# Optimization experiments

Hardware: AMD Instinct MI355X
Metric: run time of the kernel (lower is better)

Reference implementation:

```python
import jax, jax.numpy as jnp
import numpy as np

# Dimensions (Tacotron2-style decoder)
B, T_ENC, T_MEL, N_MEL = 32, 400, 800, 80
ENC_DIM = 768          # encoder(512) + token(256) + speaker(0)
PRENET, ATT_RNN, DEC_RNN = 256, 1024, 1024
ATT_DIM, LOC_FILT, LOC_K = 128, 32, 31


def setup_inputs() -> dict:
    key = jax.random.key(0)
    ks = iter(jax.random.split(key, 32))
    def lin(shape):  # weight stored [out, in(,k)], scaled by 1/sqrt(fan_in)
        fan_in = int(np.prod(shape[1:])) if len(shape) > 1 else shape[0]
        return jax.random.normal(next(ks), shape, jnp.float32) / np.sqrt(fan_in)
    return {
        'memory': jax.random.normal(next(ks), (B, T_ENC, ENC_DIM), jnp.float32),
        'decoder_inputs': jax.random.normal(next(ks), (B, N_MEL, T_MEL), jnp.float32),
        'f0s': jnp.zeros((B, 1, T_MEL), jnp.float32),  # include_f0=False -> unused
        'prenet_w1': lin((PRENET, N_MEL)),
        'prenet_w2': lin((PRENET, PRENET)),
        'att_wih': lin((4 * ATT_RNN, PRENET + ENC_DIM)),
        'att_whh': lin((4 * ATT_RNN, ATT_RNN)),
        'att_bih': jnp.zeros((4 * ATT_RNN,), jnp.float32),
        'att_bhh': jnp.zeros((4 * ATT_RNN,), jnp.float32),
        'q_w': lin((ATT_DIM, ATT_RNN)),
        'mem_w': lin((ATT_DIM, ENC_DIM)),
        'v_w': lin((ATT_DIM,)),
        'loc_conv_w': lin((LOC_FILT, 2, LOC_K)),
        'loc_dense_w': lin((ATT_DIM, LOC_FILT)),
        'dec_wih': lin((4 * DEC_RNN, ATT_RNN + ENC_DIM)),
        'dec_whh': lin((4 * DEC_RNN, DEC_RNN)),
        'dec_bih': jnp.zeros((4 * DEC_RNN,), jnp.float32),
        'dec_bhh': jnp.zeros((4 * DEC_RNN,), jnp.float32),
        'proj_w': lin((N_MEL, DEC_RNN + ENC_DIM)),
        'proj_b': jnp.zeros((N_MEL,), jnp.float32),
        'gate_w': lin((DEC_RNN + ENC_DIM,)),
        'gate_b': jnp.zeros((), jnp.float32),
        'memory_lengths': jax.random.randint(next(ks), (B,), T_ENC // 2, T_ENC + 1),
    }


def _lstm_cell(x, h, c, wih, whh, bih, bhh):
    g = x @ wih.T + bih + h @ whh.T + bhh
    i, f, gg, o = jnp.split(g, 4, axis=-1)  # torch LSTMCell gate order i,f,g,o
    c = jax.nn.sigmoid(f) * c + jax.nn.sigmoid(i) * jnp.tanh(gg)
    h = jax.nn.sigmoid(o) * jnp.tanh(c)
    return h, c


def reference(memory, decoder_inputs, f0s, prenet_w1, prenet_w2,
              att_wih, att_whh, att_bih, att_bhh, q_w, mem_w, v_w,
              loc_conv_w, loc_dense_w, dec_wih, dec_whh, dec_bih, dec_bhh,
              proj_w, proj_b, gate_w, gate_b, memory_lengths):
    # include_f0=False: f0s ignored. Dropout disabled (p=0, deterministic),
    # p_teacher_forcing=1.0 -> always teacher-force, n_frames_per_step=1.
    mask = jnp.arange(T_ENC)[None, :] >= memory_lengths[:, None]  # [B,T_enc]
    pmem = jnp.einsum('bte,ae->bta', memory, mem_w)               # processed_memory

    # parse_decoder_inputs + go frame + prenet (teacher-forced inputs)
    frames = jnp.transpose(decoder_inputs, (2, 0, 1))             # [T_mel,B,N_MEL]
    frames = jnp.concatenate([jnp.zeros((1, B, N_MEL), frames.dtype), frames], 0)
    pre = jax.nn.relu(frames @ prenet_w1.T)
    pre = jax.nn.relu(pre @ prenet_w2.T)                          # [T_mel+1,B,PRENET]
    xs = pre[:T_MEL]

    def step(carry, x):
        ah, ac, dh, dc, aw, awc, ctx = carry
        ah, ac = _lstm_cell(jnp.concatenate([x, ctx], -1), ah, ac,
                            att_wih, att_whh, att_bih, att_bhh)
        awcat = jnp.stack([aw, awc], axis=1)                      # [B,2,T_enc]
        loc = jax.lax.conv_general_dilated(
            awcat, loc_conv_w, (1,), [(LOC_K // 2, LOC_K // 2)],
            dimension_numbers=('NCH', 'OIH', 'NCH'))              # [B,LOC_FILT,T_enc]
        ploc = jnp.einsum('bft,af->bta', loc, loc_dense_w)        # [B,T_enc,ATT_DIM]
        pq = ah @ q_w.T                                           # [B,ATT_DIM]
        e = jnp.tanh(pq[:, None, :] + pmem + ploc) @ v_w          # [B,T_enc]
        e = jnp.where(mask, -1e9, e)
        aw = jax.nn.softmax(e, axis=-1)
        ctx = jnp.einsum('bt,bte->be', aw, memory)
        awc = awc + aw
        dh, dc = _lstm_cell(jnp.concatenate([ah, ctx], -1), dh, dc,
                            dec_wih, dec_whh, dec_bih, dec_bhh)
        dha = jnp.concatenate([dh, ctx], axis=1)
        mel = dha @ proj_w.T + proj_b                             # [B,N_MEL]
        gate = dha @ gate_w + gate_b                              # [B]
        return (ah, ac, dh, dc, aw, awc, ctx), (mel, gate, aw)

    f32 = memory.dtype
    carry0 = (jnp.zeros((B, ATT_RNN), f32), jnp.zeros((B, ATT_RNN), f32),
              jnp.zeros((B, DEC_RNN), f32), jnp.zeros((B, DEC_RNN), f32),
              jnp.zeros((B, T_ENC), f32), jnp.zeros((B, T_ENC), f32),
              jnp.zeros((B, ENC_DIM), f32))
    _, (mels, gates, aligns) = jax.lax.scan(step, carry0, xs)
    mel_outputs = jnp.transpose(mels, (1, 2, 0))                  # [B,N_MEL,T_mel]
    gate_outputs = gates.T                                        # [B,T_mel]
    alignments = jnp.transpose(aligns, (1, 0, 2))                 # [B,T_mel,T_enc]
    return mel_outputs, gate_outputs, alignments
```

## Files before the change

kernel.cpp:

```cpp
#include <hip/hip_runtime.h>
#include <hip/hip_fp16.h>
#include <math.h>

#define TENC 400
#define TMEL 800
#define NMEL 80
#define ENCD 768
#define PRE  256
#define ARNN 1024
#define DRNN 1024
#define ATTD 128
#define NBLK 256
#define SLOT 32

typedef unsigned uint32;

__device__ __forceinline__ float4 ld4(const float* p){ return *(const float4*)p; }
__device__ __forceinline__ float sigmf(float x){ return 1.f/(1.f + __expf(-x)); }

__device__ __forceinline__ float ld_c(const float* p){
  union { unsigned u; float f; } c;
  c.u = __hip_atomic_load((const unsigned*)p, __ATOMIC_RELAXED, __HIP_MEMORY_SCOPE_AGENT);
  return c.f;
}
__device__ __forceinline__ void st_c(float* p, float v){
  union { unsigned u; float f; } c; c.f = v;
  __hip_atomic_store((unsigned*)p, c.u, __ATOMIC_RELAXED, __HIP_MEMORY_SCOPE_AGENT);
}
__device__ __forceinline__ float4 ld4_c(const float* p){
  union { unsigned long long u[2]; float4 f; } c;
  c.u[0] = __hip_atomic_load((const unsigned long long*)p, __ATOMIC_RELAXED,
                             __HIP_MEMORY_SCOPE_AGENT);
  c.u[1] = __hip_atomic_load((const unsigned long long*)(p+2), __ATOMIC_RELAXED,
                             __HIP_MEMORY_SCOPE_AGENT);
  return c.f;
}
__device__ __forceinline__ void st2_c(float* p, float a, float b){
  union { unsigned long long u; float f[2]; } c; c.f[0]=a; c.f[1]=b;
  __hip_atomic_store((unsigned long long*)p, c.u, __ATOMIC_RELAXED,
                     __HIP_MEMORY_SCOPE_AGENT);
}
__device__ __forceinline__ uint32 ald(const uint32* p){
  return __hip_atomic_load(p, __ATOMIC_RELAXED, __HIP_MEMORY_SCOPE_AGENT);
}
__device__ __forceinline__ void ast(uint32* p, uint32 v){
  __hip_atomic_store(p, v, __ATOMIC_RELAXED, __HIP_MEMORY_SCOPE_AGENT);
}

__device__ __forceinline__ void xbar(uint32* arr, uint32* relx, uint32 ph,
                                     int xcc, int role)
{
  __syncthreads();
  int tid = threadIdx.x;
  if (tid == 0) {
    asm volatile("s_waitcnt vmcnt(0)" ::: "memory");
    ast(arr + (xcc*32 + role)*SLOT, ph);
  }
  __syncthreads();
  if (role == 0) {
    if (tid < 32) {
      while (ald(arr + (xcc*32 + tid)*SLOT) < ph) __builtin_amdgcn_s_sleep(1);
    }
    __syncthreads();
    if (tid == 0) ast(relx + xcc*SLOT, ph);
  } else if (tid == 0) {
    while (ald(relx + xcc*SLOT) < ph) __builtin_amdgcn_s_sleep(1);
  }
  __syncthreads();
}

__device__ __forceinline__ void gbar8(uint32* arr, uint32* relg, uint32 ph,
                                      int xcc, int role)
{
  __syncthreads();
  int tid = threadIdx.x;
  int bl = role >> 3;
  if (tid == 0) {
    asm volatile("s_waitcnt vmcnt(0)" ::: "memory");
    ast(arr + (xcc*32 + role)*SLOT, ph);
  }
  __syncthreads();
  if ((role & 7) == 0) {
    if (tid < 8) {
      while (ald(arr + (xcc*32 + bl*8 + tid)*SLOT) < ph) __builtin_amdgcn_s_sleep(1);
    }
    __syncthreads();
    if (tid == 0) ast(relg + (xcc*4 + bl)*SLOT, ph);
  } else if (tid == 0) {
    while (ald(relg + (xcc*4 + bl)*SLOT) < ph) __builtin_amdgcn_s_sleep(1);
  }
  __syncthreads();
}

__global__ __launch_bounds__(256) void prenet_kernel(
    const float* __restrict__ din, const float* __restrict__ w1,
    const float* __restrict__ w2, float* __restrict__ xsT)
{
  int t = blockIdx.x;
  __shared__ float f_s[32*80];
  __shared__ float p_s[32*257];
  for (int id = threadIdx.x; id < 32*80; id += 256) {
    int b = id / 80, m = id - b*80;
    f_s[id] = (t == 0) ? 0.f : din[b*(NMEL*TMEL) + m*TMEL + (t-1)];
  }
  __syncthreads();
  for (int b = 0; b < 32; ++b) {
    int k = threadIdx.x;
    float acc = 0.f;
    #pragma unroll 4
    for (int m = 0; m < 80; ++m) acc += f_s[b*80+m] * w1[k*80+m];
    p_s[b*257+k] = fmaxf(acc, 0.f);
  }
  __syncthreads();
  int b = threadIdx.x & 31, jslot = threadIdx.x >> 5;
  for (int jj = 0; jj < 32; ++jj) {
    int j = jslot*32 + jj;
    const float* w2r = w2 + j*256;
    float acc = 0.f;
    #pragma unroll 4
    for (int kk = 0; kk < 256; ++kk) acc += p_s[b*257+kk] * w2r[kk];
    xsT[(size_t)t*8192 + j*32 + b] = fmaxf(acc, 0.f);
  }
}

__global__ __launch_bounds__(256) void pmem_kernel(
  const float* __restrict__ mem, const float* __restrict__ mw, __half* __restrict__ pm16)
{
  int b = blockIdx.y, tc = blockIdx.x;
  int a = threadIdx.x & 127, th = threadIdx.x >> 7;
  for (int i = 0; i < 8; ++i) {
    int tt = tc*16 + th + 2*i;
    const float* mrow = mem + (size_t)b*(TENC*ENCD) + (size_t)tt*ENCD;
    const float* wrow = mw + a*ENCD;
    float acc = 0.f;
    #pragma unroll 4
    for (int e4 = 0; e4 < ENCD; e4 += 4) {
      float4 mv = ld4(mrow+e4), wv = ld4(wrow+e4);
      acc += mv.x*wv.x + mv.y*wv.y + mv.z*wv.z + mv.w*wv.w;
    }
    pm16[b*(TENC*ATTD) + tt*ATTD + a] = __float2half(acc);
  }
}

__global__ __launch_bounds__(256) void cvt16_kernel(
  const float* __restrict__ src, __half* __restrict__ dst, int n)
{
  int i = blockIdx.x*256 + threadIdx.x;
  int st = gridDim.x*256;
  for (; i < n; i += st) dst[i] = __float2half(src[i]);
}

struct DecArgs {
  const float *xsT;
  const __half *awih16, *awhh16, *dwih16, *dwhh16, *qw16, *pm16;
  const float *abih, *abhh, *dbih, *dbhh;
  const float *cw, *ldw, *vw;
  const int*  mlen;
  const float *pw, *pb, *gw, *gb;
  const float *memory;
  float *ahX, *dhX, *ctxX, *awX, *awcX, *eX;
  float *out_mel, *out_gate, *out_align;
  uint32 *roleCtr, *arr, *relx, *relg;
};


template<int KIH>
__device__ __forceinline__ void dmaW(const __half* __restrict__ wih,
                                     const __half* __restrict__ whh,
                                     int g, int u0g, int c, char* slot, int lane)
{
  const int kk = c*128;
  const __half* base = (kk < KIH) ? wih : whh;
  const int kbase = (kk < KIH) ? kk : (kk - KIH);
  const size_t kstr = (kk < KIH) ? (size_t)KIH : (size_t)1024;
  const int r = lane >> 4, kp = lane & 15;
  const __half* src = base + (size_t)(g*1024 + u0g + r)*kstr + kbase + kp*8;
  #pragma unroll
  for (int i = 0; i < 8; ++i) {
    __builtin_amdgcn_global_load_lds(
      (const __attribute__((address_space(1))) void*)(src + (size_t)(i*4)*kstr),
      (__attribute__((address_space(3))) void*)(slot + i*1024), 16, 0, 0);
  }
}

template<int E0, int E1, bool S0W>
__device__ __forceinline__ void loadX(int c, int lane, int b0,
  const float* __restrict__ s0, const float* __restrict__ s1,
  const float* __restrict__ s2, float4& xlo, float4& xhi)
{
  int k0 = c*128 + lane*2;
  if (S0W && c < E0) {
    xlo = ld4_c(s0 + (size_t)k0*32 + b0);
    xhi = ld4_c(s0 + (size_t)(k0+1)*32 + b0);
  } else if (c < E0) {
    xlo = ld4_c(s0 + (size_t)k0*4);
    xhi = ld4_c(s0 + (size_t)k0*4 + 4);
  } else if (c < E1) {
    int kb = k0 - E0*128;
    xlo = ld4_c(s1 + (size_t)kb*4);
    xhi = ld4_c(s1 + (size_t)kb*4 + 4);
  } else {
    int kb = k0 - E1*128;
    xlo = ld4_c(s2 + (size_t)kb*4);
    xhi = ld4_c(s2 + (size_t)kb*4 + 4);
  }
}

__device__ __forceinline__ void compW(const char* slot, int lane,
                                      float4 xlo, float4 xhi, float* acc)
{
  #pragma unroll
  for (int u = 0; u < 32; ++u) {
    __half2 w2 = *(const __half2*)(slot + u*256 + lane*4);
    float2 wf = __half22float2(w2);
    acc[u*4+0] += wf.x*xlo.x + wf.y*xhi.x;
    acc[u*4+1] += wf.x*xlo.y + wf.y*xhi.y;
    acc[u*4+2] += wf.x*xlo.z + wf.y*xhi.z;
    acc[u*4+3] += wf.x*xlo.w + wf.y*xhi.w;
  }
}

#define RS_ROUND(m, n) { bool hi = (lane & m) != 0; \
  _Pragma("unroll") for (int i = 0; i < n; ++i) { \
    float v = hi ? acc[i] : acc[i+n]; \
    float o = __shfl_xor(v, m); \
    acc[i] = (hi ? acc[i+n] : acc[i]) + o; } }

#define SBAR() __builtin_amdgcn_sched_barrier(0)
#define WAITV12() { asm volatile("s_waitcnt vmcnt(12)" ::: "memory"); SBAR(); }
#define WAITV0()  { asm volatile("s_waitcnt vmcnt(0)"  ::: "memory"); SBAR(); }
#define WAITL0()  { asm volatile("s_waitcnt lgkmcnt(0)" ::: "memory"); SBAR(); }

template<int NC, int E0, int E1, int KIH, bool S0W>
__device__ void gemm_stream(const __half* __restrict__ wih,
                            const __half* __restrict__ whh,
                            int u0g, int b0,
                            const float* __restrict__ s0,
                            const float* __restrict__ s1,
                            const float* __restrict__ s2,
                            char* ringAll, float* G)
{
  const int tid = threadIdx.x;
  const int g = tid >> 6, lane = tid & 63;
  char* slot0 = ringAll + g*16384;
  char* slot1 = slot0 + 8192;
  float acc[128];
  #pragma unroll
  for (int i = 0; i < 128; ++i) acc[i] = 0.f;

  float4 xa0, xa1, xb0, xb1;
  dmaW<KIH>(wih, whh, g, u0g, 0, slot0, lane); SBAR();
  loadX<E0,E1,S0W>(0, lane, b0, s0, s1, s2, xa0, xa1); SBAR();
  dmaW<KIH>(wih, whh, g, u0g, 1, slot1, lane); SBAR();
  loadX<E0,E1,S0W>(1, lane, b0, s0, s1, s2, xb0, xb1); SBAR();

  #pragma unroll 1
  for (int c = 0; c + 2 < NC; c += 2) {
    WAITV12();
    compW(slot0, lane, xa0, xa1, acc);
    WAITL0();
    dmaW<KIH>(wih, whh, g, u0g, c+2, slot0, lane); SBAR();
    loadX<E0,E1,S0W>(c+2, lane, b0, s0, s1, s2, xa0, xa1); SBAR();
    WAITV12();
    compW(slot1, lane, xb0, xb1, acc);
    WAITL0();
    dmaW<KIH>(wih, whh, g, u0g, c+3, slot1, lane); SBAR();
    loadX<E0,E1,S0W>(c+3, lane, b0, s0, s1, s2, xb0, xb1); SBAR();
  }
  WAITV12();
  compW(slot0, lane, xa0, xa1, acc);
  WAITV0();
  compW(slot1, lane, xb0, xb1, acc);

  RS_ROUND(32,64) RS_ROUND(16,32) RS_ROUND(8,16)
  RS_ROUND(4,8)   RS_ROUND(2,4)   RS_ROUND(1,2)
  {
    int pidx = lane*2;
    int u = pidx >> 2, b = pidx & 3;
    *(float2*)(G + g*128 + u*4 + b) = make_float2(acc[0], acc[1]);
  }
}

__device__ __forceinline__ void cell_x(const float* G, int u0g,
  const float* __restrict__ bih, const float* __restrict__ bhh,
  float& creg, float* hbuf, float* __restrict__ hXw)
{
  int tid = threadIdx.x;
  __syncthreads();
  if (tid < 128) {
    int u = tid >> 2, b = tid & 3;
    int uu = u0g + u;
    float gi = G[0*128 + u*4+b] + bih[uu]        + bhh[uu];
    float gf = G[1*128 + u*4+b] + bih[1024+uu]   + bhh[1024+uu];
    float gg = G[2*128 + u*4+b] + bih[2048+uu]   + bhh[2048+uu];
    float go = G[3*128 + u*4+b] + bih[3072+uu]   + bhh[3072+uu];
    float cn = sigmf(gf)*creg + sigmf(gi)*tanhf(gg);
    creg = cn;
    hbuf[tid] = sigmf(go)*tanhf(cn);
  }
  __syncthreads();
  if (tid < 32) {
    float4 hv = *(float4*)(hbuf + tid*4);
    st2_c(hXw + (size_t)(u0g + tid)*4,     hv.x, hv.y);
    st2_c(hXw + (size_t)(u0g + tid)*4 + 2, hv.z, hv.w);
  }
  __syncthreads();
}

__device__ void proj_x(int role, int xcc, int t,
  const float* __restrict__ dhR, const float* __restrict__ ctxX, const DecArgs& p)
{
  int tid = threadIdx.x;
  int w = tid >> 6, lane = tid & 63;
  int base = role*10 + (role < 4 ? role : 4);
  int cnt  = (role < 4) ? 11 : 10;
  for (int i = w; i < cnt; i += 4) {
    int d = base + i;
    int bl = d / 81, r = d - bl*81;
    const float* wr = (r < 80) ? (p.pw + (size_t)r*1792) : p.gw;
    float a = 0.f;
    #pragma unroll 4
    for (int ii = 0; ii < 28; ++ii) {
      int k = lane + ii*64;
      float x = (k < 1024) ? ld_c(dhR + (size_t)k*4 + bl)
                           : ld_c(ctxX + (size_t)(k-1024)*4 + bl);
      a += x * wr[k];
    }
    #pragma unroll
    for (int m = 32; m >= 1; m >>= 1) a += __shfl_xor(a, m);
    if (lane == 0) {
      int b = xcc*4 + bl;
      if (r < 80) p.out_mel[((size_t)b*80 + r)*TMEL + t] = a + p.pb[r];
      else        p.out_gate[(size_t)b*TMEL + t]         = a + p.gb[0];
    }
  }
}

__device__ void energies_x(int bl, int c8, int xcc, const DecArgs& p,
  const float* __restrict__ ahW, const float* __restrict__ awXl,
  const float* __restrict__ awcXl, float* __restrict__ eXl, float* scr)
{
  int t0 = c8*50;
  float* ah_s  = scr;
  float* pq_s  = scr + 1024;
  float* part  = scr + 1152;
  float* aw_s  = scr + 1408;
  float* awc_s = scr + 1488;
  float* loc_s = scr + 1568;
  float* epart = scr + 3218;
  int tid = threadIdx.x;
  #pragma unroll
  for (int i = 0; i < 4; ++i) {
    int u = tid + i*256;
    ah_s[u] = ld_c(ahW + (size_t)u*4 + bl);
  }
  if (tid >= 96) {
    int i = tid - 96;
    int h = (i < 80) ? i : i - 80;
    bool isC = i >= 80;
    int gidx = t0 - 15 + h;
    float v = (gidx >= 0 && gidx < TENC)
            ? (isC ? ld_c(awcXl + gidx) : ld_c(awXl + gidx)) : 0.f;
    if (isC) awc_s[h] = v; else aw_s[h] = v;
  }
  __syncthreads();
  {
    int a = tid & 127, kh = tid >> 7;
    const __half* qr = p.qw16 + (size_t)a*1024 + kh*512;
    const float*  ar = ah_s + kh*512;
    float acc = 0.f;
    for (int k = 0; k < 512; k += 8) {
      uint4 hv = *(const uint4*)(qr + k);
      const __half2* h2 = (const __half2*)&hv;
      #pragma unroll
      for (int q = 0; q < 4; ++q) {
        float2 wf = __half22float2(h2[q]);
        acc += ar[k+q*2]*wf.x + ar[k+q*2+1]*wf.y;
      }
    }
    part[tid] = acc;
  }
  __syncthreads();
  if (tid < 128) pq_s[tid] = part[tid] + part[tid+128];
  for (int id = tid; id < 50*32; id += 256) {
    int tl = id >> 5, f = id & 31;
    const float* w0 = p.cw + f*62;
    float acc = 0.f;
    #pragma unroll
    for (int k = 0; k < 31; ++k)
      acc += aw_s[tl+k]*w0[k] + awc_s[tl+k]*w0[31+k];
    loc_s[tl*33 + f] = acc;
  }
  __syncthreads();
  if (tid < 200) {
    int tl = tid >> 2, qa = tid & 3;
    int tt = t0 + tl;
    const __half* pm = p.pm16 + (size_t)(xcc*4+bl)*(TENC*ATTD) + (size_t)tt*ATTD;
    float s = 0.f;
    for (int a = qa*32; a < qa*32 + 32; ++a) {
      const float* lw = p.ldw + a*32;
      float pl = 0.f;
      #pragma unroll 8
      for (int f = 0; f < 32; ++f) pl += loc_s[tl*33 + f] * lw[f];
      s += p.vw[a] * tanhf(pq_s[a] + __half2float(pm[a]) + pl);
    }
    epart[tl*4 + qa] = s;
  }
  __syncthreads();
  if (tid < 50) {
    int tt = t0 + tid;
    float v = epart[tid*4] + epart[tid*4+1] + epart[tid*4+2] + epart[tid*4+3];
    if (tt >= p.mlen[xcc*4+bl]) v = -1000000000.0f;
    st_c(eXl + tt, v);
  }
}

__device__ void smctx_x(int bl, int jc, int xcc, int t, const DecArgs& p,
  const float* __restrict__ eXl, float* __restrict__ awXl, float* __restrict__ awcXl,
  float* __restrict__ ctxX, const __half2* mem_s, float* scr)
{
  float* red   = scr;
  float* aw_s  = scr + 256;
  float* cpart = scr + 656;
  int tid = threadIdx.x;
  float v0 = ld_c(eXl + tid);
  float v1 = (tid + 256 < TENC) ? ld_c(eXl + tid + 256) : -3.0e38f;
  red[tid] = fmaxf(v0, v1); __syncthreads();
  for (int s = 128; s > 0; s >>= 1) {
    if (tid < s) red[tid] = fmaxf(red[tid], red[tid+s]);
    __syncthreads();
  }
  float mx = red[0]; __syncthreads();
  float p0 = __expf(v0 - mx);
  float p1 = (tid + 256 < TENC) ? __expf(v1 - mx) : 0.f;
  red[tid] = p0 + p1; __syncthreads();
  for (int s = 128; s > 0; s >>= 1) {
    if (tid < s) red[tid] += red[tid+s];
    __syncthreads();
  }
  float inv = 1.f / red[0];
  aw_s[tid] = p0 * inv;
  if (tid + 256 < TENC) aw_s[tid + 256] = p1 * inv;
  __syncthreads();
  if (tid < 192) {
    int jp = tid % 48, h = tid / 48;
    float ax = 0.f, ay = 0.f;
    for (int tt = h*100; tt < h*100 + 100; ++tt) {
      float av = aw_s[tt];
      float2 m = __half22float2(mem_s[tt*48 + jp]);
      ax += av * m.x; ay += av * m.y;
    }
    cpart[(h*48 + jp)*2]     = ax;
    cpart[(h*48 + jp)*2 + 1] = ay;
  }
  __syncthreads();
  if (tid < 48) {
    float sx = cpart[tid*2]        + cpart[(48+tid)*2]
             + cpart[(96+tid)*2]   + cpart[(144+tid)*2];
    float sy = cpart[tid*2+1]      + cpart[(48+tid)*2+1]
             + cpart[(96+tid)*2+1] + cpart[(144+tid)*2+1];
    int j = jc*96 + tid*2;
    st_c(ctxX + (size_t)j*4 + bl, sx);
    st_c(ctxX + (size_t)(j+1)*4 + bl, sy);
  }
  if (jc == 0) {
    for (int i = tid; i < TENC; i += 256) {
      float a = aw_s[i];
      st_c(awXl + i, a);
      st_c(awcXl + i, ld_c(awcXl + i) + a);
      p.out_align[((size_t)(xcc*4+bl)*TMEL + t)*TENC + i] = a;
    }
  }
}

__global__ __launch_bounds__(256, 1) void decoder_loop(DecArgs p)
{
  __shared__ __align__(16) char Wring[65536];
  __shared__ __half2 mem_s[400*48];
  __shared__ float G[512];
  __shared__ float hbuf[128];
  __shared__ int s_xcc, s_role;
  int tid = threadIdx.x;
  float* scr = (float*)Wring;

  if (tid == 0) {
    uint32 x;
    asm volatile("s_getreg_b32 %0, hwreg(HW_REG_XCC_ID)" : "=s"(x));
    int xc = (int)(x & 7);
    s_xcc = xc;
    s_role = (int)atomicAdd(&p.roleCtr[xc], 1u);
  }
  __syncthreads();
  const int xcc = s_xcc, role = s_role & 31;
  const int u0g = role*32;
  const int bl = role >> 3, jc = role & 7;
  const int b0 = xcc*4;

  float* ctxX  = p.ctxX + (size_t)xcc*3072;
  float* awXl  = p.awX  + (size_t)xcc*1600 + bl*400;
  float* awcXl = p.awcX + (size_t)xcc*1600 + bl*400;
  float* eXl   = p.eX   + (size_t)xcc*1600 + bl*400;

  {
    const float* mb = p.memory + (size_t)(b0+bl)*(TENC*ENCD);
    int j0 = jc*96;
    for (int idx = tid; idx < 400*48; idx += 256) {
      int tt = idx / 48, jp = idx - tt*48;
      mem_s[idx] = __floats2half2_rn(mb[(size_t)tt*ENCD + j0 + jp*2],
                                     mb[(size_t)tt*ENCD + j0 + jp*2 + 1]);
    }
  }
  float cA = 0.f, cD = 0.f;
  uint32 ph = 0;
  __syncthreads();

  for (int t = 0; t < TMEL; ++t) {
    const float* ahR = p.ahX + (size_t)((t+1)&1)*32768 + (size_t)xcc*4096;
    float*       ahW = p.ahX + (size_t)(t&1)*32768     + (size_t)xcc*4096;
    const float* dhR = p.dhX + (size_t)((t+1)&1)*32768 + (size_t)xcc*4096;
    float*       dhW = p.dhX + (size_t)(t&1)*32768     + (size_t)xcc*4096;

    if (t > 0) proj_x(role, xcc, t-1, dhR, ctxX, p);
    gemm_stream<16, 2, 8, 1024, true>(p.awih16, p.awhh16, u0g, b0,
        p.xsT + (size_t)t*8192, ctxX, ahR, Wring, G);
    cell_x(G, u0g, p.abih, p.abhh, cA, hbuf, ahW);
    xbar(p.arr, p.relx, ++ph, xcc, role);

    energies_x(bl, jc, xcc, p, ahW, awXl, awcXl, eXl, scr);
    gbar8(p.arr, p.relg, ++ph, xcc, role);

    smctx_x(bl, jc, xcc, t, p, eXl, awXl, awcXl, ctxX, mem_s, scr);
    xbar(p.arr, p.relx, ++ph, xcc, role);

    gemm_stream<22, 8, 14, 1792, false>(p.dwih16, p.dwhh16, u0g, 0,
        ahW, ctxX, dhR, Wring, G);
    cell_x(G, u0g, p.dbih, p.dbhh, cD, hbuf, dhW);
    xbar(p.arr, p.relx, ++ph, xcc, role);
  }

  proj_x(role, xcc, TMEL-1,
         p.dhX + (size_t)((TMEL-1)&1)*32768 + (size_t)xcc*4096, ctxX, p);
}

extern "C" void kernel_launch(void* const* d_in, const int* in_sizes, int n_in,
                              void* d_out, int out_size, void* d_ws, size_t ws_size,
                              hipStream_t stream)
{
  const float* memory = (const float*)d_in[0];
  const float* din    = (const float*)d_in[1];
  const float* w1     = (const float*)d_in[3];
  const float* w2     = (const float*)d_in[4];
  const float* awih   = (const float*)d_in[5];
  const float* awhh   = (const float*)d_in[6];
  const float* abih   = (const float*)d_in[7];
  const float* abhh   = (const float*)d_in[8];
  const float* q_w    = (const float*)d_in[9];
  const float* mem_w  = (const float*)d_in[10];
  const float* v_w    = (const float*)d_in[11];
  const float* cw     = (const float*)d_in[12];
  const float* ldw    = (const float*)d_in[13];
  const float* dwih   = (const float*)d_in[14];
  const float* dwhh   = (const float*)d_in[15];
  const float* dbih   = (const float*)d_in[16];
  const float* dbhh   = (const float*)d_in[17];
  const float* pw     = (const float*)d_in[18];
  const float* pb     = (const float*)d_in[19];
  const float* gw     = (const float*)d_in[20];
  const float* gb     = (const float*)d_in[21];
  const int*   mlen   = (const int*)d_in[22];

  float* p = (float*)d_ws;
  float* xsT    = p;              p += 800*256*32;
  __half* awih16 = (__half*)p;    p += 2097152;
  __half* awhh16 = (__half*)p;    p += 2097152;
  __half* dwih16 = (__half*)p;    p += 3670016;
  __half* dwhh16 = (__half*)p;    p += 2097152;
  __half* qw16   = (__half*)p;    p += 65536;
  __half* pm16   = (__half*)p;    p += 819200;
  float* zs      = p;
  uint32* roleCtr = (uint32*)p;   p += 8;
  uint32* arr    = (uint32*)p;    p += 256*SLOT;
  uint32* relx   = (uint32*)p;    p += 8*SLOT;
  uint32* relg   = (uint32*)p;    p += 32*SLOT;
  float* ahX     = p;             p += 2*8*1024*4;
  float* dhX     = p;             p += 2*8*1024*4;
  float* ctxX    = p;             p += 8*768*4;
  float* awX     = p;             p += 8*4*400;
  float* awcX    = p;             p += 8*4*400;
  float* eX      = p;             p += 8*4*400;
  size_t zcount  = (size_t)(p - zs);

  float* out_mel   = (float*)d_out;
  float* out_gate  = out_mel + 32*80*800;
  float* out_align = out_gate + 32*800;

  hipMemsetAsync(zs, 0, zcount*sizeof(float), stream);
  prenet_kernel<<<TMEL, 256, 0, stream>>>(din, w1, w2, xsT);
  pmem_kernel<<<dim3(25,32), 256, 0, stream>>>(memory, mem_w, pm16);
  cvt16_kernel<<<256, 256, 0, stream>>>(q_w, qw16, 128*1024);
  cvt16_kernel<<<2048, 256, 0, stream>>>(awih, awih16, 4096*1024);
  cvt16_kernel<<<2048, 256, 0, stream>>>(awhh, awhh16, 4096*1024);
  cvt16_kernel<<<2048, 256, 0, stream>>>(dwih, dwih16, 4096*1792);
  cvt16_kernel<<<2048, 256, 0, stream>>>(dwhh, dwhh16, 4096*1024);

  DecArgs a;
  a.xsT = xsT;
  a.awih16 = awih16; a.awhh16 = awhh16; a.dwih16 = dwih16; a.dwhh16 = dwhh16;
  a.qw16 = qw16; a.pm16 = pm16;
  a.abih = abih; a.abhh = abhh; a.dbih = dbih; a.dbhh = dbhh;
  a.cw = cw; a.ldw = ldw; a.vw = v_w; a.mlen = mlen;
  a.pw = pw; a.pb = pb; a.gw = gw; a.gb = gb;
  a.memory = memory;
  a.ahX = ahX; a.dhX = dhX; a.ctxX = ctxX; a.awX = awX; a.awcX = awcX; a.eX = eX;
  a.out_mel = out_mel; a.out_gate = out_gate; a.out_align = out_align;
  a.roleCtr = roleCtr; a.arr = arr; a.relx = relx; a.relg = relg;

  decoder_loop<<<NBLK, 256, 0, stream>>>(a);
}
```

Measured before the change: 113.8 ms.

## Triple-buffer LSTM weight and activation streaming via LDS DMA, move memory slice to global

The LSTM gemm stream changes from a two-slot ring with activation vectors in registers to a three-slot LDS ring. Both the fp16 weight chunk and the activation chunk are now fetched with global_load_lds, and the code waits on vmcnt before each compute step, so two chunks are in flight while one is consumed. To free LDS for the larger ring, the per-block half-precision memory slice is no longer staged in shared memory. A separate pre-kernel now writes it to global workspace, and the context computation reads it from global/L2 every step. The deeper prefetch is meant to hide weight-fetch latency. The cost is extra global traffic in the context stage and a relaxed-atomic load path replaced by plain DMA loads of cross-block data, whose coherence may differ.

New measurement: 130.8 ms. 1.15x slower.

```diff
diff --git a/kernel.cpp b/kernel.cpp
--- a/kernel.cpp
+++ b/kernel.cpp
@@ -26,14 +26,6 @@
 __device__ __forceinline__ void st_c(float* p, float v){
   union { unsigned u; float f; } c; c.f = v;
   __hip_atomic_store((unsigned*)p, c.u, __ATOMIC_RELAXED, __HIP_MEMORY_SCOPE_AGENT);
-}
-__device__ __forceinline__ float4 ld4_c(const float* p){
-  union { unsigned long long u[2]; float4 f; } c;
-  c.u[0] = __hip_atomic_load((const unsigned long long*)p, __ATOMIC_RELAXED,
-                             __HIP_MEMORY_SCOPE_AGENT);
-  c.u[1] = __hip_atomic_load((const unsigned long long*)(p+2), __ATOMIC_RELAXED,
-                             __HIP_MEMORY_SCOPE_AGENT);
-  return c.f;
 }
 __device__ __forceinline__ void st2_c(float* p, float a, float b){
   union { unsigned long long u; float f[2]; } c; c.f[0]=a; c.f[1]=b;
@@ -142,6 +134,19 @@
   }
 }
 
+__global__ __launch_bounds__(256) void mem16_kernel(
+  const float* __restrict__ mem, __half2* __restrict__ m16)
+{
+  int b = blockIdx.y, jc = blockIdx.x;
+  const float* mb = mem + (size_t)b*(TENC*ENCD) + jc*96;
+  __half2* dst = m16 + ((size_t)(b*8 + jc))*19200;
+  for (int idx = threadIdx.x; idx < 19200; idx += 256) {
+    int tt = idx / 48, jp = idx - tt*48;
+    dst[idx] = __floats2half2_rn(mb[(size_t)tt*ENCD + jp*2],
+                                 mb[(size_t)tt*ENCD + jp*2 + 1]);
+  }
+}
+
 __global__ __launch_bounds__(256) void cvt16_kernel(
   const float* __restrict__ src, __half* __restrict__ dst, int n)
 {
@@ -153,16 +158,21 @@
 struct DecArgs {
   const float *xsT;
   const __half *awih16, *awhh16, *dwih16, *dwhh16, *qw16, *pm16;
+  const __half2 *mem16;
   const float *abih, *abhh, *dbih, *dbhh;
   const float *cw, *ldw, *vw;
   const int*  mlen;
   const float *pw, *pb, *gw, *gb;
-  const float *memory;
   float *ahX, *dhX, *ctxX, *awX, *awcX, *eX;
   float *out_mel, *out_gate, *out_align;
   uint32 *roleCtr, *arr, *relx, *relg;
 };
 
+
+#define SBAR() __builtin_amdgcn_sched_barrier(0)
+#define WAITV20() { asm volatile("s_waitcnt vmcnt(20)" ::: "memory"); SBAR(); }
+#define WAITV10() { asm volatile("s_waitcnt vmcnt(10)" ::: "memory"); SBAR(); }
+#define WAITV0()  { asm volatile("s_waitcnt vmcnt(0)"  ::: "memory"); SBAR(); }
 
 template<int KIH>
 __device__ __forceinline__ void dmaW(const __half* __restrict__ wih,
@@ -184,31 +194,29 @@
 }
 
 template<int E0, int E1, bool S0W>
-__device__ __forceinline__ void loadX(int c, int lane, int b0,
+__device__ __forceinline__ void dmaX(int c, int lane, int b0,
   const float* __restrict__ s0, const float* __restrict__ s1,
-  const float* __restrict__ s2, float4& xlo, float4& xhi)
-{
-  int k0 = c*128 + lane*2;
-  if (S0W && c < E0) {
-    xlo = ld4_c(s0 + (size_t)k0*32 + b0);
-    xhi = ld4_c(s0 + (size_t)(k0+1)*32 + b0);
-  } else if (c < E0) {
-    xlo = ld4_c(s0 + (size_t)k0*4);
-    xhi = ld4_c(s0 + (size_t)k0*4 + 4);
-  } else if (c < E1) {
-    int kb = k0 - E0*128;
-    xlo = ld4_c(s1 + (size_t)kb*4);
-    xhi = ld4_c(s1 + (size_t)kb*4 + 4);
-  } else {
-    int kb = k0 - E1*128;
-    xlo = ld4_c(s2 + (size_t)kb*4);
-    xhi = ld4_c(s2 + (size_t)kb*4 + 4);
-  }
-}
-
-__device__ __forceinline__ void compW(const char* slot, int lane,
-                                      float4 xlo, float4 xhi, float* acc)
-{
+  const float* __restrict__ s2, char* slot)
+{
+  #pragma unroll
+  for (int j = 0; j < 2; ++j) {
+    int k = c*128 + j*64 + lane;
+    const float* src;
+    if (S0W && c < E0)      src = s0 + (size_t)k*32 + b0;
+    else if (c < E0)        src = s0 + (size_t)k*4;
+    else if (c < E1)        src = s1 + (size_t)(k - E0*128)*4;
+    else                    src = s2 + (size_t)(k - E1*128)*4;
+    __builtin_amdgcn_global_load_lds(
+      (const __attribute__((address_space(1))) void*)src,
+      (__attribute__((address_space(3))) void*)(slot + 8192 + j*1024 + lane*16),
+      16, 0, 1);
+  }
+}
+
+__device__ __forceinline__ void compW(const char* slot, int lane, float* acc)
+{
+  float4 xlo = *(const float4*)(slot + 8192 + lane*32);
+  float4 xhi = *(const float4*)(slot + 8192 + lane*32 + 16);
   #pragma unroll
   for (int u = 0; u < 32; ++u) {
     __half2 w2 = *(const __half2*)(slot + u*256 + lane*4);
@@ -226,11 +234,6 @@
     float o = __shfl_xor(v, m); \
     acc[i] = (hi ? acc[i+n] : acc[i]) + o; } }
 
-#define SBAR() __builtin_amdgcn_sched_barrier(0)
-#define WAITV12() { asm volatile("s_waitcnt vmcnt(12)" ::: "memory"); SBAR(); }
-#define WAITV0()  { asm volatile("s_waitcnt vmcnt(0)"  ::: "memory"); SBAR(); }
-#define WAITL0()  { asm volatile("s_waitcnt lgkmcnt(0)" ::: "memory"); SBAR(); }
-
 template<int NC, int E0, int E1, int KIH, bool S0W>
 __device__ void gemm_stream(const __half* __restrict__ wih,
                             const __half* __restrict__ whh,
@@ -242,35 +245,34 @@
 {
   const int tid = threadIdx.x;
   const int g = tid >> 6, lane = tid & 63;
-  char* slot0 = ringAll + g*16384;
-  char* slot1 = slot0 + 8192;
+  char* ring = ringAll + g*30720;
   float acc[128];
   #pragma unroll
   for (int i = 0; i < 128; ++i) acc[i] = 0.f;
 
-  float4 xa0, xa1, xb0, xb1;
-  dmaW<KIH>(wih, whh, g, u0g, 0, slot0, lane); SBAR();
-  loadX<E0,E1,S0W>(0, lane, b0, s0, s1, s2, xa0, xa1); SBAR();
-  dmaW<KIH>(wih, whh, g, u0g, 1, slot1, lane); SBAR();
-  loadX<E0,E1,S0W>(1, lane, b0, s0, s1, s2, xb0, xb1); SBAR();
-
+  dmaW<KIH>(wih, whh, g, u0g, 0, ring, lane);
+  dmaX<E0,E1,S0W>(0, lane, b0, s0, s1, s2, ring);
+  dmaW<KIH>(wih, whh, g, u0g, 1, ring + 10240, lane);
+  dmaX<E0,E1,S0W>(1, lane, b0, s0, s1, s2, ring + 10240);
+  SBAR();
+
+  int sc = 0, sp = 2;
   #pragma unroll 1
-  for (int c = 0; c + 2 < NC; c += 2) {
-    WAITV12();
-    compW(slot0, lane, xa0, xa1, acc);
-    WAITL0();
-    dmaW<KIH>(wih, whh, g, u0g, c+2, slot0, lane); SBAR();
-    loadX<E0,E1,S0W>(c+2, lane, b0, s0, s1, s2, xa0, xa1); SBAR();
-    WAITV12();
-    compW(slot1, lane, xb0, xb1, acc);
-    WAITL0();
-    dmaW<KIH>(wih, whh, g, u0g, c+3, slot1, lane); SBAR();
-    loadX<E0,E1,S0W>(c+3, lane, b0, s0, s1, s2, xb0, xb1); SBAR();
-  }
-  WAITV12();
-  compW(slot0, lane, xa0, xa1, acc);
-  WAITV0();
-  compW(slot1, lane, xb0, xb1, acc);
+  for (int c = 0; c < NC; ++c) {
+    if (c + 2 < NC) {
+      char* ps = ring + sp*10240;
+      dmaW<KIH>(wih, whh, g, u0g, c+2, ps, lane);
+      dmaX<E0,E1,S0W>(c+2, lane, b0, s0, s1, s2, ps);
+      SBAR();
+    }
+    if (c + 2 < NC)      { WAITV20(); }
+    else if (c + 1 < NC) { WAITV10(); }
+    else                 { WAITV0();  }
+    compW(ring + sc*10240, lane, acc);
+    SBAR();
+    sc = (sc+1 == 3) ? 0 : sc+1;
+    sp = (sp+1 == 3) ? 0 : sp+1;
+  }
 
   RS_ROUND(32,64) RS_ROUND(16,32) RS_ROUND(8,16)
   RS_ROUND(4,8)   RS_ROUND(2,4)   RS_ROUND(1,2)
@@ -417,7 +419,7 @@
 
 __device__ void smctx_x(int bl, int jc, int xcc, int t, const DecArgs& p,
   const float* __restrict__ eXl, float* __restrict__ awXl, float* __restrict__ awcXl,
-  float* __restrict__ ctxX, const __half2* mem_s, float* scr)
+  float* __restrict__ ctxX, const __half2* __restrict__ mslice, float* scr)
 {
   float* red   = scr;
   float* aw_s  = scr + 256;
@@ -447,7 +449,7 @@
     float ax = 0.f, ay = 0.f;
     for (int tt = h*100; tt < h*100 + 100; ++tt) {
       float av = aw_s[tt];
-      float2 m = __half22float2(mem_s[tt*48 + jp]);
+      float2 m = __half22float2(mslice[tt*48 + jp]);
       ax += av * m.x; ay += av * m.y;
     }
     cpart[(h*48 + jp)*2]     = ax;
@@ -475,8 +477,7 @@
 
 __global__ __launch_bounds__(256, 1) void decoder_loop(DecArgs p)
 {
-  __shared__ __align__(16) char Wring[65536];
-  __shared__ __half2 mem_s[400*48];
+  __shared__ __align__(16) char Wring[122880];
   __shared__ float G[512];
   __shared__ float hbuf[128];
   __shared__ int s_xcc, s_role;
@@ -500,19 +501,10 @@
   float* awXl  = p.awX  + (size_t)xcc*1600 + bl*400;
   float* awcXl = p.awcX + (size_t)xcc*1600 + bl*400;
   float* eXl   = p.eX   + (size_t)xcc*1600 + bl*400;
-
-  {
-    const float* mb = p.memory + (size_t)(b0+bl)*(TENC*ENCD);
-    int j0 = jc*96;
-    for (int idx = tid; idx < 400*48; idx += 256) {
-      int tt = idx / 48, jp = idx - tt*48;
-      mem_s[idx] = __floats2half2_rn(mb[(size_t)tt*ENCD + j0 + jp*2],
-                                     mb[(size_t)tt*ENCD + j0 + jp*2 + 1]);
-    }
-  }
+  const __half2* mslice = p.mem16 + ((size_t)((xcc*4+bl)*8 + jc))*19200;
+
   float cA = 0.f, cD = 0.f;
   uint32 ph = 0;
-  __syncthreads();
 
   for (int t = 0; t < TMEL; ++t) {
     const float* ahR = p.ahX + (size_t)((t+1)&1)*32768 + (size_t)xcc*4096;
@@ -529,7 +521,7 @@
     energies_x(bl, jc, xcc, p, ahW, awXl, awcXl, eXl, scr);
     gbar8(p.arr, p.relg, ++ph, xcc, role);
 
-    smctx_x(bl, jc, xcc, t, p, eXl, awXl, awcXl, ctxX, mem_s, scr);
+    smctx_x(bl, jc, xcc, t, p, eXl, awXl, awcXl, ctxX, mslice, scr);
     xbar(p.arr, p.relx, ++ph, xcc, role);
 
     gemm_stream<22, 8, 14, 1792, false>(p.dwih16, p.dwhh16, u0g, 0,
@@ -577,6 +569,7 @@
   __half* dwhh16 = (__half*)p;    p += 2097152;
   __half* qw16   = (__half*)p;    p += 65536;
   __half* pm16   = (__half*)p;    p += 819200;
+  __half2* mem16 = (__half2*)p;   p += 4915200;
   float* zs      = p;
   uint32* roleCtr = (uint32*)p;   p += 8;
   uint32* arr    = (uint32*)p;    p += 256*SLOT;
@@ -597,6 +590,7 @@
   hipMemsetAsync(zs, 0, zcount*sizeof(float), stream);
   prenet_kernel<<<TMEL, 256, 0, stream>>>(din, w1, w2, xsT);
   pmem_kernel<<<dim3(25,32), 256, 0, stream>>>(memory, mem_w, pm16);
+  mem16_kernel<<<dim3(8,32), 256, 0, stream>>>(memory, mem16);
   cvt16_kernel<<<256, 256, 0, stream>>>(q_w, qw16, 128*1024);
   cvt16_kernel<<<2048, 256, 0, stream>>>(awih, awih16, 4096*1024);
   cvt16_kernel<<<2048, 256, 0, stream>>>(awhh, awhh16, 4096*1024);
@@ -606,11 +600,10 @@
   DecArgs a;
   a.xsT = xsT;
   a.awih16 = awih16; a.awhh16 = awhh16; a.dwih16 = dwih16; a.dwhh16 = dwhh16;
-  a.qw16 = qw16; a.pm16 = pm16;
+  a.qw16 = qw16; a.pm16 = pm16; a.mem16 = mem16;
   a.abih = abih; a.abhh = abhh; a.dbih = dbih; a.dbhh = dbhh;
   a.cw = cw; a.ldw = ldw; a.vw = v_w; a.mlen = mlen;
   a.pw = pw; a.pb = pb; a.gw = gw; a.gb = gb;
-  a.memory = memory;
   a.ahX = ahX; a.dhX = dhX; a.ctxX = ctxX; a.awX = awX; a.awcX = awcX; a.eX = eX;
   a.out_mel = out_mel; a.out_gate = out_gate; a.out_align = out_align;
   a.roleCtr = roleCtr; a.arr = arr; a.relx = relx; a.relg = relg;
```

## Deepen weight-streaming ring to triple buffering and move memory slice out of LDS

Applied to the files above, without the earlier changes.

The LSTM weight-streaming GEMM goes from a two-slot LDS ring to a three-slot ring, so two chunks of weight DMA are in flight while one is computed, with the vmcnt waits adjusted to match. To make LDS room, the per-block fp16 memory slice for the context computation is no longer held in shared memory. It is precomputed once by a new kernel into global workspace and read from there each step. This trades LDS-resident context reads for global/L2 reads in smctx in exchange for deeper latency hiding in the dominant weight-streaming phases.

New measurement: 137.7 ms. 1.21x slower.

```diff
diff --git a/kernel.cpp b/kernel.cpp
--- a/kernel.cpp
+++ b/kernel.cpp
@@ -142,6 +142,19 @@
   }
 }
 
+__global__ __launch_bounds__(256) void mem16_kernel(
+  const float* __restrict__ mem, __half2* __restrict__ m16)
+{
+  int b = blockIdx.y, jc = blockIdx.x;
+  const float* mb = mem + (size_t)b*(TENC*ENCD) + jc*96;
+  __half2* dst = m16 + ((size_t)(b*8 + jc))*19200;
+  for (int idx = threadIdx.x; idx < 19200; idx += 256) {
+    int tt = idx / 48, jp = idx - tt*48;
+    dst[idx] = __floats2half2_rn(mb[(size_t)tt*ENCD + jp*2],
+                                 mb[(size_t)tt*ENCD + jp*2 + 1]);
+  }
+}
+
 __global__ __launch_bounds__(256) void cvt16_kernel(
   const float* __restrict__ src, __half* __restrict__ dst, int n)
 {
@@ -153,16 +166,21 @@
 struct DecArgs {
   const float *xsT;
   const __half *awih16, *awhh16, *dwih16, *dwhh16, *qw16, *pm16;
+  const __half2 *mem16;
   const float *abih, *abhh, *dbih, *dbhh;
   const float *cw, *ldw, *vw;
   const int*  mlen;
   const float *pw, *pb, *gw, *gb;
-  const float *memory;
   float *ahX, *dhX, *ctxX, *awX, *awcX, *eX;
   float *out_mel, *out_gate, *out_align;
   uint32 *roleCtr, *arr, *relx, *relg;
 };
 
+#define SBAR() __builtin_amdgcn_sched_barrier(0)
+#define WAITV24() { asm volatile("s_waitcnt vmcnt(24)" ::: "memory"); SBAR(); }
+#define WAITV16() { asm volatile("s_waitcnt vmcnt(16)" ::: "memory"); SBAR(); }
+#define WAITV0()  { asm volatile("s_waitcnt vmcnt(0)"  ::: "memory"); SBAR(); }
+#define WAITL0()  { asm volatile("s_waitcnt lgkmcnt(0)" ::: "memory"); SBAR(); }
 
 template<int KIH>
 __device__ __forceinline__ void dmaW(const __half* __restrict__ wih,
@@ -226,11 +244,6 @@
     float o = __shfl_xor(v, m); \
     acc[i] = (hi ? acc[i+n] : acc[i]) + o; } }
 
-#define SBAR() __builtin_amdgcn_sched_barrier(0)
-#define WAITV12() { asm volatile("s_waitcnt vmcnt(12)" ::: "memory"); SBAR(); }
-#define WAITV0()  { asm volatile("s_waitcnt vmcnt(0)"  ::: "memory"); SBAR(); }
-#define WAITL0()  { asm volatile("s_waitcnt lgkmcnt(0)" ::: "memory"); SBAR(); }
-
 template<int NC, int E0, int E1, int KIH, bool S0W>
 __device__ void gemm_stream(const __half* __restrict__ wih,
                             const __half* __restrict__ whh,
@@ -242,35 +255,39 @@
 {
   const int tid = threadIdx.x;
   const int g = tid >> 6, lane = tid & 63;
-  char* slot0 = ringAll + g*16384;
-  char* slot1 = slot0 + 8192;
+  char* ring = ringAll + g*24576;
   float acc[128];
   #pragma unroll
   for (int i = 0; i < 128; ++i) acc[i] = 0.f;
 
   float4 xa0, xa1, xb0, xb1;
-  dmaW<KIH>(wih, whh, g, u0g, 0, slot0, lane); SBAR();
-  loadX<E0,E1,S0W>(0, lane, b0, s0, s1, s2, xa0, xa1); SBAR();
-  dmaW<KIH>(wih, whh, g, u0g, 1, slot1, lane); SBAR();
-  loadX<E0,E1,S0W>(1, lane, b0, s0, s1, s2, xb0, xb1); SBAR();
-
+  dmaW<KIH>(wih, whh, g, u0g, 0, ring, lane);            SBAR();
+  loadX<E0,E1,S0W>(0, lane, b0, s0, s1, s2, xa0, xa1);   SBAR();
+  dmaW<KIH>(wih, whh, g, u0g, 1, ring + 8192, lane);     SBAR();
+  loadX<E0,E1,S0W>(1, lane, b0, s0, s1, s2, xb0, xb1);   SBAR();
+  dmaW<KIH>(wih, whh, g, u0g, 2, ring + 16384, lane);    SBAR();
+
+  int sc = 0;
   #pragma unroll 1
-  for (int c = 0; c + 2 < NC; c += 2) {
-    WAITV12();
-    compW(slot0, lane, xa0, xa1, acc);
-    WAITL0();
-    dmaW<KIH>(wih, whh, g, u0g, c+2, slot0, lane); SBAR();
-    loadX<E0,E1,S0W>(c+2, lane, b0, s0, s1, s2, xa0, xa1); SBAR();
-    WAITV12();
-    compW(slot1, lane, xb0, xb1, acc);
-    WAITL0();
-    dmaW<KIH>(wih, whh, g, u0g, c+3, slot1, lane); SBAR();
-    loadX<E0,E1,S0W>(c+3, lane, b0, s0, s1, s2, xb0, xb1); SBAR();
-  }
-  WAITV12();
-  compW(slot0, lane, xa0, xa1, acc);
-  WAITV0();
-  compW(slot1, lane, xb0, xb1, acc);
+  for (int c = 0; c < NC; ++c) {
+    if (c + 2 < NC)      { WAITV24(); }
+    else if (c + 1 < NC) { WAITV16(); }
+    else                 { WAITV0();  }
+    if (c & 1) compW(ring + sc*8192, lane, xb0, xb1, acc);
+    else       compW(ring + sc*8192, lane, xa0, xa1, acc);
+    SBAR();
+    if (c + 2 < NC) {
+      if (c & 1) loadX<E0,E1,S0W>(c+2, lane, b0, s0, s1, s2, xb0, xb1);
+      else       loadX<E0,E1,S0W>(c+2, lane, b0, s0, s1, s2, xa0, xa1);
+      SBAR();
+    }
+    if (c + 3 < NC) {
+      WAITL0();
+      dmaW<KIH>(wih, whh, g, u0g, c+3, ring + sc*8192, lane);
+      SBAR();
+    }
+    sc = (sc+1 == 3) ? 0 : sc+1;
+  }
 
   RS_ROUND(32,64) RS_ROUND(16,32) RS_ROUND(8,16)
   RS_ROUND(4,8)   RS_ROUND(2,4)   RS_ROUND(1,2)
@@ -417,7 +434,7 @@
 
 __device__ void smctx_x(int bl, int jc, int xcc, int t, const DecArgs& p,
   const float* __restrict__ eXl, float* __restrict__ awXl, float* __restrict__ awcXl,
-  float* __restrict__ ctxX, const __half2* mem_s, float* scr)
+  float* __restrict__ ctxX, const __half2* __restrict__ mslice, float* scr)
 {
   float* red   = scr;
   float* aw_s  = scr + 256;
@@ -447,7 +464,7 @@
     float ax = 0.f, ay = 0.f;
     for (int tt = h*100; tt < h*100 + 100; ++tt) {
       float av = aw_s[tt];
-      float2 m = __half22float2(mem_s[tt*48 + jp]);
+      float2 m = __half22float2(mslice[tt*48 + jp]);
       ax += av * m.x; ay += av * m.y;
     }
     cpart[(h*48 + jp)*2]     = ax;
@@ -475,13 +492,12 @@
 
 __global__ __launch_bounds__(256, 1) void decoder_loop(DecArgs p)
 {
-  __shared__ __align__(16) char Wring[65536];
-  __shared__ __half2 mem_s[400*48];
+  __shared__ __align__(16) char Wring[98304];
+  __shared__ __align__(16) float scr_s[3424];
   __shared__ float G[512];
   __shared__ float hbuf[128];
   __shared__ int s_xcc, s_role;
   int tid = threadIdx.x;
-  float* scr = (float*)Wring;
 
   if (tid == 0) {
     uint32 x;
@@ -500,19 +516,10 @@
   float* awXl  = p.awX  + (size_t)xcc*1600 + bl*400;
   float* awcXl = p.awcX + (size_t)xcc*1600 + bl*400;
   float* eXl   = p.eX   + (size_t)xcc*1600 + bl*400;
-
-  {
-    const float* mb = p.memory + (size_t)(b0+bl)*(TENC*ENCD);
-    int j0 = jc*96;
-    for (int idx = tid; idx < 400*48; idx += 256) {
-      int tt = idx / 48, jp = idx - tt*48;
-      mem_s[idx] = __floats2half2_rn(mb[(size_t)tt*ENCD + j0 + jp*2],
-                                     mb[(size_t)tt*ENCD + j0 + jp*2 + 1]);
-    }
-  }
+  const __half2* mslice = p.mem16 + ((size_t)((xcc*4+bl)*8 + jc))*19200;
+
   float cA = 0.f, cD = 0.f;
   uint32 ph = 0;
-  __syncthreads();
 
   for (int t = 0; t < TMEL; ++t) {
     const float* ahR = p.ahX + (size_t)((t+1)&1)*32768 + (size_t)xcc*4096;
@@ -526,10 +533,10 @@
     cell_x(G, u0g, p.abih, p.abhh, cA, hbuf, ahW);
     xbar(p.arr, p.relx, ++ph, xcc, role);
 
-    energies_x(bl, jc, xcc, p, ahW, awXl, awcXl, eXl, scr);
+    energies_x(bl, jc, xcc, p, ahW, awXl, awcXl, eXl, scr_s);
     gbar8(p.arr, p.relg, ++ph, xcc, role);
 
-    smctx_x(bl, jc, xcc, t, p, eXl, awXl, awcXl, ctxX, mem_s, scr);
+    smctx_x(bl, jc, xcc, t, p, eXl, awXl, awcXl, ctxX, mslice, scr_s);
     xbar(p.arr, p.relx, ++ph, xcc, role);
 
     gemm_stream<22, 8, 14, 1792, false>(p.dwih16, p.dwhh16, u0g, 0,
@@ -577,6 +584,7 @@
   __half* dwhh16 = (__half*)p;    p += 2097152;
   __half* qw16   = (__half*)p;    p += 65536;
   __half* pm16   = (__half*)p;    p += 819200;
+  __half2* mem16 = (__half2*)p;   p += 4915200;
   float* zs      = p;
   uint32* roleCtr = (uint32*)p;   p += 8;
   uint32* arr    = (uint32*)p;    p += 256*SLOT;
@@ -597,6 +605,7 @@
   hipMemsetAsync(zs, 0, zcount*sizeof(float), stream);
   prenet_kernel<<<TMEL, 256, 0, stream>>>(din, w1, w2, xsT);
   pmem_kernel<<<dim3(25,32), 256, 0, stream>>>(memory, mem_w, pm16);
+  mem16_kernel<<<dim3(8,32), 256, 0, stream>>>(memory, mem16);
   cvt16_kernel<<<256, 256, 0, stream>>>(q_w, qw16, 128*1024);
   cvt16_kernel<<<2048, 256, 0, stream>>>(awih, awih16, 4096*1024);
   cvt16_kernel<<<2048, 256, 0, stream>>>(awhh, awhh16, 4096*1024);
@@ -606,11 +615,10 @@
   DecArgs a;
   a.xsT = xsT;
   a.awih16 = awih16; a.awhh16 = awhh16; a.dwih16 = dwih16; a.dwhh16 = dwhh16;
-  a.qw16 = qw16; a.pm16 = pm16;
+  a.qw16 = qw16; a.pm16 = pm16; a.mem16 = mem16;
   a.abih = abih; a.abhh = abhh; a.dbih = dbih; a.dbhh = dbhh;
   a.cw = cw; a.ldw = ldw; a.vw = v_w; a.mlen = mlen;
   a.pw = pw; a.pb = pb; a.gw = gw; a.gb = gb;
-  a.memory = memory;
   a.ahX = ahX; a.dhX = dhX; a.ctxX = ctxX; a.awX = awX; a.awcX = awcX; a.eX = eX;
   a.out_mel = out_mel; a.out_gate = out_gate; a.out_align = out_align;
   a.roleCtr = roleCtr; a.arr = arr; a.relx = relx; a.relg = relg;
```
